# Kernel optimization log

Hardware: AMD Instinct MI355X
Metric: run time of the kernel (lower is better)

The kernel has to match this reference:

```python
import jax, jax.numpy as jnp
import numpy as np


def setup_inputs() -> dict:
    key = jax.random.key(0)
    ks = jax.random.split(key, 7)
    B, N, Fin, Fout = 32, 1024, 64, 64
    s = 1.0 / np.sqrt(Fin)
    return {
        "X": jax.random.normal(ks[0], (B, N, Fin), dtype=jnp.float32),
        "A": jax.random.normal(ks[1], (B, N, N), dtype=jnp.float32),  # unused in forward, kept for signature fidelity
        "W": jax.random.uniform(ks[2], (Fin, Fout), jnp.float32, -s, s),
        "att_W": jax.random.uniform(ks[3], (Fin, Fout), jnp.float32, -s, s),
        "a": jax.random.uniform(ks[4], (Fout, Fout), jnp.float32, -s, s),
        "bias_W": jax.random.uniform(ks[5], (Fout,), jnp.float32, -s, s),
        "self_W": jax.random.uniform(ks[6], (Fin, Fout), jnp.float32, -s, s),
    }


def reference(X, A, W, att_W, a, bias_W, self_W):
    # att_X = X @ att_W : [B, N, Fout]
    att_X = jnp.einsum('bnf,fg->bng', X, att_W)
    # torch einsum 'ij,ajk->ajk' sums `a` over i => per-feature scale a.sum(0)
    scale = jnp.sum(a, axis=0)  # [Fout]
    # Z[b,i,k] = sum_j att_X[b,i,j] * scale[j] * att_X[b,k,j]  -> [B, N, N]
    Z = jnp.einsum('big,bkg->bik', att_X * scale, att_X)
    n = Z.shape[1]
    Z = Z * (1.0 - jnp.eye(n, dtype=Z.dtype))  # zero diagonal per batch
    att = jax.nn.leaky_relu(Z, negative_slope=0.01)
    # H = att @ (X W) + bias_W + X self_W
    XW = jnp.einsum('bnf,fg->bng', X, W)
    H = jnp.einsum('bnm,bmg->bng', att, XW) + bias_W
    H = H + jnp.einsum('bnf,fg->bng', X, self_W)
    return H
```

## Files before the change

### kernel.cpp

```cpp
#include <hip/hip_runtime.h>

#define DEV __device__ __forceinline__
typedef short s16x8 __attribute__((ext_vector_type(8)));
typedef float f32x16 __attribute__((ext_vector_type(16)));
typedef unsigned short u16;

#define WAIT_VMCNT(N) asm volatile("s_waitcnt vmcnt(" #N ")" ::: "memory")
#define CFENCE asm volatile("" ::: "memory")

DEV unsigned cvt_pk_bf16(float lo, float hi) {
  unsigned r;
  asm volatile("v_cvt_pk_bf16_f32 %0, %1, %2" : "=v"(r) : "v"(lo), "v"(hi));
  return r;
}
DEV u16 f2bf(float f) {
  unsigned u = __builtin_bit_cast(unsigned, f);
  unsigned r = u + 0x7fffu + ((u >> 16) & 1u);
  return (u16)(r >> 16);
}
DEV float bf2f(u16 u) { return __builtin_bit_cast(float, (unsigned)u << 16); }
DEV f32x16 zero16() {
  f32x16 v;
  #pragma unroll
  for (int i = 0; i < 16; ++i) v[i] = 0.f;
  return v;
}

DEV void gld16(const u16* g, u16* l) {
  __builtin_amdgcn_global_load_lds(
      (const __attribute__((address_space(1))) void*)g,
      (__attribute__((address_space(3))) void*)l, 16, 0, 0);
}

DEV void stage_tile64(const u16* __restrict__ gbase, size_t stride, u16* lbuf, int t) {
  #pragma unroll
  for (int p = 0; p < 2; ++p) {
    int c = p * 256 + t;
    int row = c >> 3, s = c & 7;
    int gck = s ^ (row & 7);
    const u16* src = gbase + (size_t)row * stride + gck * 8;
    u16* dst = lbuf + (size_t)(p * 256 + (t & 192)) * 8;
    gld16(src, dst);
  }
}

DEV s16x8 frag(const u16* buf, int row, int chunk) {
  return *(const s16x8*)(buf + row * 64 + ((chunk ^ (row & 7)) << 3));
}

DEV void stage_wt(const float* __restrict__ src, u16* dst, int t) {
  #pragma unroll
  for (int r = 0; r < 4; ++r) {
    int e = (r * 256 + t) * 4;
    int f = e >> 6, g0 = e & 63;
    float4 v = *(const float4*)(src + f * 64 + g0);
    float vv[4] = {v.x, v.y, v.z, v.w};
    #pragma unroll
    for (int j = 0; j < 4; ++j) {
      int g = g0 + j;
      dst[g * 64 + ((((f >> 3) ^ (g & 7)) << 3) | (f & 7))] = f2bf(vv[j]);
    }
  }
}

__global__ __launch_bounds__(256) void prep_kernel(
    const float* __restrict__ X, const float* __restrict__ W,
    const float* __restrict__ attW, const float* __restrict__ Aa,
    const float* __restrict__ biasW, const float* __restrict__ selfW,
    u16* __restrict__ Kbf, u16* __restrict__ Vt, u16* __restrict__ Bb,
    float* __restrict__ scal_ws) {
  __shared__ __align__(16) u16 Xl[128 * 64];
  __shared__ __align__(16) u16 Wt[3][64 * 64];
  __shared__ float sc4[4][64];
  __shared__ __align__(16) u16 Kl[128 * 64];
  __shared__ __align__(16) u16 Bl[128 * 64];
  __shared__ __align__(16) u16 Vl[64 * 136];

  const int t = threadIdx.x;
  const int r0 = blockIdx.x * 128;
  const int b = r0 >> 10;
  const int n0 = r0 & 1023;

  {
    int qt = t >> 6, d = t & 63;
    float s = 0.f;
    #pragma unroll
    for (int i = 0; i < 16; ++i) s += Aa[(qt * 16 + i) * 64 + d];
    sc4[qt][d] = s;
  }

  #pragma unroll
  for (int r = 0; r < 4; ++r) {
    int e = (r * 256 + t) * 8;
    int row = e >> 6;
    int chunk = (e >> 3) & 7;
    const float4* src = (const float4*)(X + (size_t)(r0 + row) * 64 + chunk * 8);
    float4 a0 = src[0], a1 = src[1];
    unsigned* dst = (unsigned*)&Xl[row * 64 + ((chunk ^ (row & 7)) << 3)];
    dst[0] = cvt_pk_bf16(a0.x, a0.y);
    dst[1] = cvt_pk_bf16(a0.z, a0.w);
    dst[2] = cvt_pk_bf16(a1.x, a1.y);
    dst[3] = cvt_pk_bf16(a1.z, a1.w);
  }
  stage_wt(attW, &Wt[0][0], t);
  stage_wt(W, &Wt[1][0], t);
  stage_wt(selfW, &Wt[2][0], t);
  __syncthreads();

  const int lane = t & 63, w = t >> 6, h = lane >> 5, ln = lane & 31;
  const int rowbase = w * 32;

  s16x8 xa[4];
  #pragma unroll
  for (int ks = 0; ks < 4; ++ks) {
    int row = rowbase + ln;
    xa[ks] = frag(Xl, row, ks * 2 + h);
  }

  #pragma unroll
  for (int cf = 0; cf < 2; ++cf) {
    f32x16 aA = zero16(), aW = zero16(), aS = zero16();
    #pragma unroll
    for (int ks = 0; ks < 4; ++ks) {
      int g = cf * 32 + ln;
      s16x8 bA = frag(&Wt[0][0], g, ks * 2 + h);
      s16x8 bW = frag(&Wt[1][0], g, ks * 2 + h);
      s16x8 bS = frag(&Wt[2][0], g, ks * 2 + h);
      aA = __builtin_amdgcn_mfma_f32_32x32x16_bf16(xa[ks], bA, aA, 0, 0, 0);
      aW = __builtin_amdgcn_mfma_f32_32x32x16_bf16(xa[ks], bW, aW, 0, 0, 0);
      aS = __builtin_amdgcn_mfma_f32_32x32x16_bf16(xa[ks], bS, aS, 0, 0, 0);
    }
    int d = cf * 32 + ln;
    float bi = biasW[d];
    #pragma unroll
    for (int reg = 0; reg < 16; ++reg) {
      int rl = (reg & 3) + 8 * (reg >> 2) + 4 * h;
      int row = rowbase + rl;
      Kl[row * 64 + d] = f2bf(aA[reg]);
      Bl[row * 64 + d] = f2bf(aS[reg] + bi);
    }
    #pragma unroll
    for (int pg = 0; pg < 4; ++pg) {
      int n = rowbase + pg * 8 + 4 * h;
      *(unsigned*)&Vl[d * 136 + n] = cvt_pk_bf16(aW[pg * 4 + 0], aW[pg * 4 + 1]);
      *(unsigned*)&Vl[d * 136 + n + 2] = cvt_pk_bf16(aW[pg * 4 + 2], aW[pg * 4 + 3]);
    }
  }
  __syncthreads();

  #pragma unroll
  for (int pass = 0; pass < 4; ++pass) {
    int c = pass * 256 + t;
    int row = c >> 3, ck = c & 7;
    size_t go = (size_t)(r0 + row) * 64 + ck * 8;
    *(s16x8*)&Kbf[go] = *(const s16x8*)&Kl[row * 64 + ck * 8];
    *(s16x8*)&Bb[go] = *(const s16x8*)&Bl[row * 64 + ck * 8];
  }
  #pragma unroll
  for (int pass = 0; pass < 4; ++pass) {
    int c = pass * 256 + t;
    int d = c >> 4, ck = c & 15;
    *(s16x8*)&Vt[(size_t)(b * 64 + d) * 1024 + n0 + ck * 8] =
        *(const s16x8*)&Vl[d * 136 + ck * 8];
  }
  if (t < 64) scal_ws[t] = sc4[0][t] + sc4[1][t] + sc4[2][t] + sc4[3][t];
}

#define PROC(SV, DG, PWV)                                                      \
  do {                                                                         \
    float p_[16];                                                              \
    _Pragma("unroll") for (int r_ = 0; r_ < 16; ++r_) {                        \
      float v_ = (SV)[r_];                                                     \
      p_[r_] = fmaxf(v_, 0.f) + 0.01f * fminf(v_, 0.f);                        \
    }                                                                          \
    if (DG) {                                                                  \
      _Pragma("unroll") for (int r_ = 0; r_ < 16; ++r_) {                      \
        int rl_ = (r_ & 3) + 8 * (r_ >> 2) + 4 * h;                            \
        p_[r_] = (rl_ == ln) ? 0.f : p_[r_];                                   \
      }                                                                        \
    }                                                                          \
    unsigned pk_[8];                                                           \
    _Pragma("unroll") for (int i_ = 0; i_ < 8; ++i_)                           \
        pk_[i_] = cvt_pk_bf16(p_[2 * i_], p_[2 * i_ + 1]);                     \
    auto a0_ = __builtin_amdgcn_permlane32_swap(pk_[0], pk_[2], false, false); \
    auto a1_ = __builtin_amdgcn_permlane32_swap(pk_[1], pk_[3], false, false); \
    auto a2_ = __builtin_amdgcn_permlane32_swap(pk_[4], pk_[6], false, false); \
    auto a3_ = __builtin_amdgcn_permlane32_swap(pk_[5], pk_[7], false, false); \
    PWV[0][0] = a0_[0]; PWV[0][1] = a1_[0]; PWV[0][2] = a0_[1];                \
    PWV[0][3] = a1_[1]; PWV[1][0] = a2_[0]; PWV[1][1] = a3_[0];                \
    PWV[1][2] = a2_[1]; PWV[1][3] = a3_[1];                                    \
  } while (0)

__global__ __launch_bounds__(256) void attn_kernel(
    const u16* __restrict__ Kbf, const u16* __restrict__ Vt,
    const u16* __restrict__ Bb, const float* __restrict__ scal_ws,
    float* __restrict__ Hout) {
  __shared__ __align__(16) u16 Qla[2][64 * 64];
  __shared__ __align__(16) u16 KV[3][2][64 * 64];
  __shared__ float Ol[128 * 65];
  __shared__ float sc[64];

  const int t = threadIdx.x;
  const int b = blockIdx.x;
  const int q0 = blockIdx.y * 128;
  const int lane = t & 63, w = t >> 6, h = lane >> 5, ln = lane & 31;
  const int qrow = w * 32 + ln;

  const u16* Kg = Kbf + (size_t)b * 65536;
  const u16* Vg = Vt + (size_t)b * 65536;

  if (t < 64) sc[t] = scal_ws[t];

  stage_tile64(Kg + (size_t)q0 * 64, 64, Qla[0], t);
  stage_tile64(Kg + (size_t)(q0 + 64) * 64, 64, Qla[1], t);
  stage_tile64(Kg, 64, KV[0][0], t);
  stage_tile64(Vg, 1024, KV[0][1], t);
  WAIT_VMCNT(4);
  __builtin_amdgcn_s_barrier();
  CFENCE;

  s16x8 qf[4];
  #pragma unroll
  for (int ks = 0; ks < 4; ++ks) {
    s16x8 q = frag(Qla[w >> 1], qrow & 63, ks * 2 + h);
    union { unsigned u[4]; s16x8 v; } qq;
    #pragma unroll
    for (int j = 0; j < 4; ++j) {
      float lo = bf2f((u16)q[2 * j]) * sc[ks * 16 + h * 8 + 2 * j];
      float hi = bf2f((u16)q[2 * j + 1]) * sc[ks * 16 + h * 8 + 2 * j + 1];
      qq.u[j] = cvt_pk_bf16(lo, hi);
    }
    qf[ks] = qq.v;
  }

  f32x16 o0 = zero16(), o1 = zero16();

  #pragma unroll
  for (int tix = 0; tix < 16; ++tix) {
    const int kv0 = tix * 64;
    if (tix < 15) {
      const int ns = (tix + 1) % 3;
      stage_tile64(Kg + (size_t)(kv0 + 64) * 64, 64, KV[ns][0], t);
      stage_tile64(Vg + (kv0 + 64), 1024, KV[ns][1], t);
      WAIT_VMCNT(4);
    } else {
      WAIT_VMCNT(0);
    }
    __builtin_amdgcn_s_barrier();
    CFENCE;
    const u16* Kl = KV[tix % 3][0];
    const u16* Vl = KV[tix % 3][1];

    f32x16 s0 = zero16(), s1 = zero16();
    __builtin_amdgcn_s_setprio(1);
    #pragma unroll
    for (int ks = 0; ks < 4; ++ks) {
      s0 = __builtin_amdgcn_mfma_f32_32x32x16_bf16(frag(Kl, ln, ks * 2 + h), qf[ks], s0, 0, 0, 0);
      s1 = __builtin_amdgcn_mfma_f32_32x32x16_bf16(frag(Kl, 32 + ln, ks * 2 + h), qf[ks], s1, 0, 0, 0);
    }
    __builtin_amdgcn_s_setprio(0);

    const bool dg0 = (kv0 == q0 + w * 32);
    const bool dg1 = (kv0 + 32 == q0 + w * 32);
    unsigned pw0[2][4], pw1[2][4];
    PROC(s0, dg0, pw0);
    PROC(s1, dg1, pw1);

    __builtin_amdgcn_s_setprio(1);
    #pragma unroll
    for (int kk = 0; kk < 4; ++kk) {
      union { unsigned u[4]; s16x8 v; } pb;
      pb.u[0] = (kk < 2 ? pw0 : pw1)[kk & 1][0];
      pb.u[1] = (kk < 2 ? pw0 : pw1)[kk & 1][1];
      pb.u[2] = (kk < 2 ? pw0 : pw1)[kk & 1][2];
      pb.u[3] = (kk < 2 ? pw0 : pw1)[kk & 1][3];
      o0 = __builtin_amdgcn_mfma_f32_32x32x16_bf16(frag(Vl, ln, kk * 2 + h), pb.v, o0, 0, 0, 0);
      o1 = __builtin_amdgcn_mfma_f32_32x32x16_bf16(frag(Vl, 32 + ln, kk * 2 + h), pb.v, o1, 0, 0, 0);
    }
    __builtin_amdgcn_s_setprio(0);
  }

  #pragma unroll
  for (int reg = 0; reg < 16; ++reg) {
    int dd = (reg & 3) + 8 * (reg >> 2) + 4 * h;
    Ol[(w * 32 + ln) * 65 + dd] = o0[reg];
    Ol[(w * 32 + ln) * 65 + 32 + dd] = o1[reg];
  }
  __syncthreads();
  #pragma unroll
  for (int i = 0; i < 8; ++i) {
    int fi = i * 256 + t;
    int q = fi >> 4, dw = (fi & 15) * 4;
    float4 v = {Ol[q * 65 + dw], Ol[q * 65 + dw + 1], Ol[q * 65 + dw + 2], Ol[q * 65 + dw + 3]};
    size_t go = ((size_t)b * 1024 + q0 + q) * 64 + dw;
    const short4 bv = *(const short4*)(Bb + go);
    v.x += bf2f((u16)bv.x);
    v.y += bf2f((u16)bv.y);
    v.z += bf2f((u16)bv.z);
    v.w += bf2f((u16)bv.w);
    *(float4*)(Hout + go) = v;
  }
}

extern "C" void kernel_launch(void* const* d_in, const int* in_sizes, int n_in,
                              void* d_out, int out_size, void* d_ws, size_t ws_size,
                              hipStream_t stream) {
  const float* X = (const float*)d_in[0];
  const float* W = (const float*)d_in[2];
  const float* attW = (const float*)d_in[3];
  const float* a = (const float*)d_in[4];
  const float* biasW = (const float*)d_in[5];
  const float* selfW = (const float*)d_in[6];
  float* H = (float*)d_out;

  u16* Kbf = (u16*)d_ws;
  u16* Vt = Kbf + (size_t)32 * 1024 * 64;
  u16* Bb = Vt + (size_t)32 * 1024 * 64;
  float* scal = (float*)(Bb + (size_t)32 * 1024 * 64);

  prep_kernel<<<256, 256, 0, stream>>>(X, W, attW, a, biasW, selfW, Kbf, Vt, Bb, scal);
  attn_kernel<<<dim3(32, 8), 256, 0, stream>>>(Kbf, Vt, Bb, scal, H);
}
```

Baseline: 36.31 us.

## Halve tile sizes, split KV across waves, deepen the KV pipeline

Both kernels now use 64-row tiles, which doubles the grid: prep goes to 512 blocks and attention to 32x16. In attention, the four waves split into two query halves and two KV halves. Each wave runs half the KV tile, and the two partial results are reduced through LDS at the end. A 4-buffer ring prefetches two tiles ahead, Q is loaded straight into registers, and the output staging buffer reuses the KV shared memory with a swizzled layout. The aim is to fill more CUs and hide load latency, at the cost of an extra reduction step and more total K/V tile staging.

```diff
diff --git a/kernel.cpp b/kernel.cpp
--- a/kernel.cpp
+++ b/kernel.cpp
@@ -46,6 +46,10 @@
 
 DEV s16x8 frag(const u16* buf, int row, int chunk) {
   return *(const s16x8*)(buf + row * 64 + ((chunk ^ (row & 7)) << 3));
+}
+
+DEV int kswz(int row, int d) {
+  return row * 64 + ((((d >> 3) ^ (row & 7)) << 3) | (d & 7));
 }
 
 DEV void stage_wt(const float* __restrict__ src, u16* dst, int t) {
@@ -69,19 +73,18 @@
     const float* __restrict__ biasW, const float* __restrict__ selfW,
     u16* __restrict__ Kbf, u16* __restrict__ Vt, u16* __restrict__ Bb,
     float* __restrict__ scal_ws) {
-  __shared__ __align__(16) u16 Xl[128 * 64];
+  __shared__ __align__(16) u16 Xl[64 * 64];
   __shared__ __align__(16) u16 Wt[3][64 * 64];
+  __shared__ __align__(16) u16 Bl[64 * 64];
+  __shared__ __align__(16) u16 Vl[64 * 72];
   __shared__ float sc4[4][64];
-  __shared__ __align__(16) u16 Kl[128 * 64];
-  __shared__ __align__(16) u16 Bl[128 * 64];
-  __shared__ __align__(16) u16 Vl[64 * 136];
 
   const int t = threadIdx.x;
-  const int r0 = blockIdx.x * 128;
+  const int r0 = blockIdx.x * 64;
   const int b = r0 >> 10;
   const int n0 = r0 & 1023;
 
-  {
+  if (blockIdx.x == 0) {
     int qt = t >> 6, d = t & 63;
     float s = 0.f;
     #pragma unroll
@@ -90,13 +93,12 @@
   }
 
   #pragma unroll
-  for (int r = 0; r < 4; ++r) {
-    int e = (r * 256 + t) * 8;
-    int row = e >> 6;
-    int chunk = (e >> 3) & 7;
-    const float4* src = (const float4*)(X + (size_t)(r0 + row) * 64 + chunk * 8);
+  for (int p = 0; p < 2; ++p) {
+    int c = p * 256 + t;
+    int row = c >> 3, ck = c & 7;
+    const float4* src = (const float4*)(X + (size_t)(r0 + row) * 64 + ck * 8);
     float4 a0 = src[0], a1 = src[1];
-    unsigned* dst = (unsigned*)&Xl[row * 64 + ((chunk ^ (row & 7)) << 3)];
+    unsigned* dst = (unsigned*)&Xl[row * 64 + ((ck ^ (row & 7)) << 3)];
     dst[0] = cvt_pk_bf16(a0.x, a0.y);
     dst[1] = cvt_pk_bf16(a0.z, a0.w);
     dst[2] = cvt_pk_bf16(a1.x, a1.y);
@@ -108,62 +110,59 @@
   __syncthreads();
 
   const int lane = t & 63, w = t >> 6, h = lane >> 5, ln = lane & 31;
-  const int rowbase = w * 32;
+  const int rg = (w >> 1) * 32;
+  const int cf = w & 1;
+  const int d = cf * 32 + ln;
 
   s16x8 xa[4];
   #pragma unroll
+  for (int ks = 0; ks < 4; ++ks) xa[ks] = frag(Xl, rg + ln, ks * 2 + h);
+
+  f32x16 aA = zero16(), aW = zero16(), aS = zero16();
+  #pragma unroll
   for (int ks = 0; ks < 4; ++ks) {
-    int row = rowbase + ln;
-    xa[ks] = frag(Xl, row, ks * 2 + h);
-  }
-
-  #pragma unroll
-  for (int cf = 0; cf < 2; ++cf) {
-    f32x16 aA = zero16(), aW = zero16(), aS = zero16();
-    #pragma unroll
-    for (int ks = 0; ks < 4; ++ks) {
-      int g = cf * 32 + ln;
-      s16x8 bA = frag(&Wt[0][0], g, ks * 2 + h);
-      s16x8 bW = frag(&Wt[1][0], g, ks * 2 + h);
-      s16x8 bS = frag(&Wt[2][0], g, ks * 2 + h);
-      aA = __builtin_amdgcn_mfma_f32_32x32x16_bf16(xa[ks], bA, aA, 0, 0, 0);
-      aW = __builtin_amdgcn_mfma_f32_32x32x16_bf16(xa[ks], bW, aW, 0, 0, 0);
-      aS = __builtin_amdgcn_mfma_f32_32x32x16_bf16(xa[ks], bS, aS, 0, 0, 0);
-    }
-    int d = cf * 32 + ln;
-    float bi = biasW[d];
-    #pragma unroll
-    for (int reg = 0; reg < 16; ++reg) {
-      int rl = (reg & 3) + 8 * (reg >> 2) + 4 * h;
-      int row = rowbase + rl;
-      Kl[row * 64 + d] = f2bf(aA[reg]);
-      Bl[row * 64 + d] = f2bf(aS[reg] + bi);
-    }
-    #pragma unroll
-    for (int pg = 0; pg < 4; ++pg) {
-      int n = rowbase + pg * 8 + 4 * h;
-      *(unsigned*)&Vl[d * 136 + n] = cvt_pk_bf16(aW[pg * 4 + 0], aW[pg * 4 + 1]);
-      *(unsigned*)&Vl[d * 136 + n + 2] = cvt_pk_bf16(aW[pg * 4 + 2], aW[pg * 4 + 3]);
-    }
+    s16x8 bA = frag(&Wt[0][0], d, ks * 2 + h);
+    s16x8 bW = frag(&Wt[1][0], d, ks * 2 + h);
+    s16x8 bS = frag(&Wt[2][0], d, ks * 2 + h);
+    aA = __builtin_amdgcn_mfma_f32_32x32x16_bf16(xa[ks], bA, aA, 0, 0, 0);
+    aW = __builtin_amdgcn_mfma_f32_32x32x16_bf16(xa[ks], bW, aW, 0, 0, 0);
+    aS = __builtin_amdgcn_mfma_f32_32x32x16_bf16(xa[ks], bS, aS, 0, 0, 0);
   }
   __syncthreads();
 
-  #pragma unroll
-  for (int pass = 0; pass < 4; ++pass) {
-    int c = pass * 256 + t;
+  const float bi = biasW[d];
+  #pragma unroll
+  for (int reg = 0; reg < 16; ++reg) {
+    int rl = (reg & 3) + 8 * (reg >> 2) + 4 * h;
+    int row = rg + rl;
+    Xl[kswz(row, d)] = f2bf(aA[reg]);
+    Bl[kswz(row, d)] = f2bf(aS[reg] + bi);
+  }
+  #pragma unroll
+  for (int pg = 0; pg < 4; ++pg) {
+    int n = rg + pg * 8 + 4 * h;
+    *(unsigned*)&Vl[d * 72 + n] = cvt_pk_bf16(aW[pg * 4 + 0], aW[pg * 4 + 1]);
+    *(unsigned*)&Vl[d * 72 + n + 2] = cvt_pk_bf16(aW[pg * 4 + 2], aW[pg * 4 + 3]);
+  }
+  __syncthreads();
+
+  #pragma unroll
+  for (int p = 0; p < 2; ++p) {
+    int c = p * 256 + t;
     int row = c >> 3, ck = c & 7;
     size_t go = (size_t)(r0 + row) * 64 + ck * 8;
-    *(s16x8*)&Kbf[go] = *(const s16x8*)&Kl[row * 64 + ck * 8];
-    *(s16x8*)&Bb[go] = *(const s16x8*)&Bl[row * 64 + ck * 8];
-  }
-  #pragma unroll
-  for (int pass = 0; pass < 4; ++pass) {
-    int c = pass * 256 + t;
-    int d = c >> 4, ck = c & 15;
-    *(s16x8*)&Vt[(size_t)(b * 64 + d) * 1024 + n0 + ck * 8] =
-        *(const s16x8*)&Vl[d * 136 + ck * 8];
-  }
-  if (t < 64) scal_ws[t] = sc4[0][t] + sc4[1][t] + sc4[2][t] + sc4[3][t];
+    *(s16x8*)&Kbf[go] = *(const s16x8*)&Xl[row * 64 + ((ck ^ (row & 7)) << 3)];
+    *(s16x8*)&Bb[go] = *(const s16x8*)&Bl[row * 64 + ((ck ^ (row & 7)) << 3)];
+  }
+  #pragma unroll
+  for (int p = 0; p < 2; ++p) {
+    int c = p * 256 + t;
+    int dd = c >> 3, ck = c & 7;
+    *(s16x8*)&Vt[(size_t)(b * 64 + dd) * 1024 + n0 + ck * 8] =
+        *(const s16x8*)&Vl[dd * 72 + ck * 8];
+  }
+  if (blockIdx.x == 0 && t < 64)
+    scal_ws[t] = sc4[0][t] + sc4[1][t] + sc4[2][t] + sc4[3][t];
 }
 
 #define PROC(SV, DG, PWV)                                                      \
@@ -195,109 +194,119 @@
     const u16* __restrict__ Kbf, const u16* __restrict__ Vt,
     const u16* __restrict__ Bb, const float* __restrict__ scal_ws,
     float* __restrict__ Hout) {
-  __shared__ __align__(16) u16 Qla[2][64 * 64];
-  __shared__ __align__(16) u16 KV[3][2][64 * 64];
-  __shared__ float Ol[128 * 65];
+  __shared__ __align__(16) u16 KV[4][2][64 * 64];
   __shared__ float sc[64];
+  float* Ol0 = (float*)&KV[0][0][0];
+  float* Ol1 = (float*)&KV[1][0][0];
 
   const int t = threadIdx.x;
   const int b = blockIdx.x;
-  const int q0 = blockIdx.y * 128;
+  const int q0 = blockIdx.y * 64;
   const int lane = t & 63, w = t >> 6, h = lane >> 5, ln = lane & 31;
-  const int qrow = w * 32 + ln;
+  const int qh = w & 1, kvh = w >> 1;
+  const int qg = q0 + qh * 32 + ln;
 
   const u16* Kg = Kbf + (size_t)b * 65536;
   const u16* Vg = Vt + (size_t)b * 65536;
 
-  if (t < 64) sc[t] = scal_ws[t];
-
-  stage_tile64(Kg + (size_t)q0 * 64, 64, Qla[0], t);
-  stage_tile64(Kg + (size_t)(q0 + 64) * 64, 64, Qla[1], t);
-  stage_tile64(Kg, 64, KV[0][0], t);
-  stage_tile64(Vg, 1024, KV[0][1], t);
-  WAIT_VMCNT(4);
+  s16x8 qraw[4];
+  #pragma unroll
+  for (int ks = 0; ks < 4; ++ks)
+    qraw[ks] = *(const s16x8*)(Kg + (size_t)qg * 64 + ks * 16 + h * 8);
+  float scv = 0.f;
+  if (t < 64) scv = scal_ws[t];
+
+  stage_tile64(Kg, 64, &KV[0][0][0], t);
+  stage_tile64(Vg, 1024, &KV[0][1][0], t);
+  stage_tile64(Kg + (size_t)64 * 64, 64, &KV[1][0][0], t);
+  stage_tile64(Vg + 64, 1024, &KV[1][1][0], t);
+
+  if (t < 64) sc[t] = scv;
+  asm volatile("s_waitcnt lgkmcnt(0)" ::: "memory");
   __builtin_amdgcn_s_barrier();
   CFENCE;
 
   s16x8 qf[4];
   #pragma unroll
   for (int ks = 0; ks < 4; ++ks) {
-    s16x8 q = frag(Qla[w >> 1], qrow & 63, ks * 2 + h);
+    float4 s0 = *(const float4*)&sc[ks * 16 + h * 8];
+    float4 s1 = *(const float4*)&sc[ks * 16 + h * 8 + 4];
     union { unsigned u[4]; s16x8 v; } qq;
-    #pragma unroll
-    for (int j = 0; j < 4; ++j) {
-      float lo = bf2f((u16)q[2 * j]) * sc[ks * 16 + h * 8 + 2 * j];
-      float hi = bf2f((u16)q[2 * j + 1]) * sc[ks * 16 + h * 8 + 2 * j + 1];
-      qq.u[j] = cvt_pk_bf16(lo, hi);
-    }
+    qq.u[0] = cvt_pk_bf16(bf2f((u16)qraw[ks][0]) * s0.x, bf2f((u16)qraw[ks][1]) * s0.y);
+    qq.u[1] = cvt_pk_bf16(bf2f((u16)qraw[ks][2]) * s0.z, bf2f((u16)qraw[ks][3]) * s0.w);
+    qq.u[2] = cvt_pk_bf16(bf2f((u16)qraw[ks][4]) * s1.x, bf2f((u16)qraw[ks][5]) * s1.y);
+    qq.u[3] = cvt_pk_bf16(bf2f((u16)qraw[ks][6]) * s1.z, bf2f((u16)qraw[ks][7]) * s1.w);
     qf[ks] = qq.v;
   }
 
   f32x16 o0 = zero16(), o1 = zero16();
 
-  #pragma unroll
+  #pragma unroll 1
   for (int tix = 0; tix < 16; ++tix) {
     const int kv0 = tix * 64;
-    if (tix < 15) {
-      const int ns = (tix + 1) % 3;
-      stage_tile64(Kg + (size_t)(kv0 + 64) * 64, 64, KV[ns][0], t);
-      stage_tile64(Vg + (kv0 + 64), 1024, KV[ns][1], t);
+    if (tix < 14) {
+      const int ns = (tix + 2) & 3;
+      stage_tile64(Kg + (size_t)(kv0 + 128) * 64, 64, &KV[ns][0][0], t);
+      stage_tile64(Vg + (kv0 + 128), 1024, &KV[ns][1][0], t);
+      WAIT_VMCNT(8);
+    } else if (tix == 14) {
       WAIT_VMCNT(4);
     } else {
       WAIT_VMCNT(0);
     }
     __builtin_amdgcn_s_barrier();
     CFENCE;
-    const u16* Kl = KV[tix % 3][0];
-    const u16* Vl = KV[tix % 3][1];
-
-    f32x16 s0 = zero16(), s1 = zero16();
+    const u16* Kl = &KV[tix & 3][0][0];
+    const u16* Vl = &KV[tix & 3][1][0];
+
+    f32x16 s = zero16();
     __builtin_amdgcn_s_setprio(1);
     #pragma unroll
-    for (int ks = 0; ks < 4; ++ks) {
-      s0 = __builtin_amdgcn_mfma_f32_32x32x16_bf16(frag(Kl, ln, ks * 2 + h), qf[ks], s0, 0, 0, 0);
-      s1 = __builtin_amdgcn_mfma_f32_32x32x16_bf16(frag(Kl, 32 + ln, ks * 2 + h), qf[ks], s1, 0, 0, 0);
+    for (int ks = 0; ks < 4; ++ks)
+      s = __builtin_amdgcn_mfma_f32_32x32x16_bf16(frag(Kl, kvh * 32 + ln, ks * 2 + h), qf[ks], s, 0, 0, 0);
+    __builtin_amdgcn_s_setprio(0);
+
+    const bool dg = (kv0 + kvh * 32) == (q0 + qh * 32);
+    unsigned pw[2][4];
+    PROC(s, dg, pw);
+
+    __builtin_amdgcn_s_setprio(1);
+    #pragma unroll
+    for (int kk = 0; kk < 2; ++kk) {
+      union { unsigned u[4]; s16x8 v; } pb;
+      pb.u[0] = pw[kk][0]; pb.u[1] = pw[kk][1];
+      pb.u[2] = pw[kk][2]; pb.u[3] = pw[kk][3];
+      int ch = kvh * 4 + kk * 2 + h;
+      o0 = __builtin_amdgcn_mfma_f32_32x32x16_bf16(frag(Vl, ln, ch), pb.v, o0, 0, 0, 0);
+      o1 = __builtin_amdgcn_mfma_f32_32x32x16_bf16(frag(Vl, 32 + ln, ch), pb.v, o1, 0, 0, 0);
     }
     __builtin_amdgcn_s_setprio(0);
-
-    const bool dg0 = (kv0 == q0 + w * 32);
-    const bool dg1 = (kv0 + 32 == q0 + w * 32);
-    unsigned pw0[2][4], pw1[2][4];
-    PROC(s0, dg0, pw0);
-    PROC(s1, dg1, pw1);
-
-    __builtin_amdgcn_s_setprio(1);
-    #pragma unroll
-    for (int kk = 0; kk < 4; ++kk) {
-      union { unsigned u[4]; s16x8 v; } pb;
-      pb.u[0] = (kk < 2 ? pw0 : pw1)[kk & 1][0];
-      pb.u[1] = (kk < 2 ? pw0 : pw1)[kk & 1][1];
-      pb.u[2] = (kk < 2 ? pw0 : pw1)[kk & 1][2];
-      pb.u[3] = (kk < 2 ? pw0 : pw1)[kk & 1][3];
-      o0 = __builtin_amdgcn_mfma_f32_32x32x16_bf16(frag(Vl, ln, kk * 2 + h), pb.v, o0, 0, 0, 0);
-      o1 = __builtin_amdgcn_mfma_f32_32x32x16_bf16(frag(Vl, 32 + ln, kk * 2 + h), pb.v, o1, 0, 0, 0);
-    }
-    __builtin_amdgcn_s_setprio(0);
-  }
-
+  }
+
+  float* Od = kvh ? Ol1 : Ol0;
+  const int q = qh * 32 + ln;
   #pragma unroll
   for (int reg = 0; reg < 16; ++reg) {
-    int dd = (reg & 3) + 8 * (reg >> 2) + 4 * h;
-    Ol[(w * 32 + ln) * 65 + dd] = o0[reg];
-    Ol[(w * 32 + ln) * 65 + 32 + dd] = o1[reg];
+    int rl = (reg & 3) + 8 * (reg >> 2) + 4 * h;
+    int d0 = rl, d1 = 32 + rl;
+    Od[q * 64 + ((((d0 >> 2) ^ (q & 15)) << 2) | (d0 & 3))] = o0[reg];
+    Od[q * 64 + ((((d1 >> 2) ^ (q & 15)) << 2) | (d1 & 3))] = o1[reg];
   }
   __syncthreads();
   #pragma unroll
-  for (int i = 0; i < 8; ++i) {
+  for (int i = 0; i < 4; ++i) {
     int fi = i * 256 + t;
-    int q = fi >> 4, dw = (fi & 15) * 4;
-    float4 v = {Ol[q * 65 + dw], Ol[q * 65 + dw + 1], Ol[q * 65 + dw + 2], Ol[q * 65 + dw + 3]};
-    size_t go = ((size_t)b * 1024 + q0 + q) * 64 + dw;
+    int qq = fi >> 4, g = fi & 15;
+    int off = qq * 64 + ((g ^ (qq & 15)) << 2);
+    float4 v0 = *(const float4*)&Ol0[off];
+    float4 v1 = *(const float4*)&Ol1[off];
+    size_t go = ((size_t)b * 1024 + q0 + qq) * 64 + g * 4;
     const short4 bv = *(const short4*)(Bb + go);
-    v.x += bf2f((u16)bv.x);
-    v.y += bf2f((u16)bv.y);
-    v.z += bf2f((u16)bv.z);
-    v.w += bf2f((u16)bv.w);
+    float4 v;
+    v.x = v0.x + v1.x + bf2f((u16)bv.x);
+    v.y = v0.y + v1.y + bf2f((u16)bv.y);
+    v.z = v0.z + v1.z + bf2f((u16)bv.z);
+    v.w = v0.w + v1.w + bf2f((u16)bv.w);
     *(float4*)(Hout + go) = v;
   }
 }
@@ -318,6 +327,6 @@
   u16* Bb = Vt + (size_t)32 * 1024 * 64;
   float* scal = (float*)(Bb + (size_t)32 * 1024 * 64);
 
-  prep_kernel<<<256, 256, 0, stream>>>(X, W, attW, a, biasW, selfW, Kbf, Vt, Bb, scal);
-  attn_kernel<<<dim3(32, 8), 256, 0, stream>>>(Kbf, Vt, Bb, scal, H);
-}
+  prep_kernel<<<512, 256, 0, stream>>>(X, W, attW, a, biasW, selfW, Kbf, Vt, Bb, scal);
+  attn_kernel<<<dim3(32, 16), 256, 0, stream>>>(Kbf, Vt, Bb, scal, H);
+}
```

Measured after the change: 35.63 us. No clear change (-1.9%).
